# Kernel optimization log

Hardware: AMD Instinct MI355X
Metric: run time of the kernel (lower is better)

The kernel has to match this reference:

```python
import jax, jax.numpy as jnp
import numpy as np


def setup_inputs() -> dict:
    key = jax.random.key(0)
    k1, k2 = jax.random.split(key)
    x1 = jax.random.normal(k1, (256, 128, 32, 32), dtype=jnp.float32)   # queries [B,C,h,w]
    x2 = jax.random.normal(k2, (16, 8, 128, 32, 32), dtype=jnp.float32)  # supports [n_way,shot,C,h,w]
    return {"x1": x1, "x2": x2}


def reference(x1, x2):
    # --- cal_covariance: per-class channel covariance over all support pixels ---
    W, S, C, h, w = x2.shape
    sup = x2.transpose(0, 2, 1, 3, 4).reshape(W, C, S * h * w)  # [W, C, S*h*w]
    sup = sup - sup.mean(axis=2, keepdims=True)
    cova = jnp.einsum('wci,wdi->wcd', sup, sup) / (S * h * w - 1)  # [W, C, C]

    # --- cal_similarity: diagonal of q^T Cova q with per-channel L2-normalized query ---
    B, C, h, w = x1.shape
    q = x1.reshape(B, C, h * w)
    q = q / jnp.linalg.norm(q, axis=2, keepdims=True)  # norm over spatial dim per channel
    # diag_i = q[:, i]^T Cova q[:, i]; compute diagonal directly (no (hw)x(hw) matrix)
    sim = jnp.einsum('bci,wcd,bdi->bwi', q, cova, q)  # [B, W, h*w]
    return sim.reshape(B, W * h * w)
```

## Files before the change

kernel.cpp:

```cpp
#include <hip/hip_runtime.h>

typedef _Float16 half8 __attribute__((ext_vector_type(8)));
typedef _Float16 half4 __attribute__((ext_vector_type(4)));
typedef float    f32x4 __attribute__((ext_vector_type(4)));

#define W_CLS 16
#define SHOT  8
#define C_CH  128
#define HW    1024
#define NSAMP (SHOT*HW)
#define B_Q   256

__device__ __forceinline__ void gload_lds16(const _Float16* g, _Float16* l) {
    __builtin_amdgcn_global_load_lds((const __attribute__((address_space(1))) unsigned int*)g,
                                     (__attribute__((address_space(3))) unsigned int*)l,
                                     16, 0, 0);
}


__global__ __launch_bounds__(512) void cova_kernel(const float* __restrict__ x2,
                                                   float* __restrict__ PG,
                                                   float* __restrict__ pmean) {
    __shared__ _Float16 XT[2][128*72];
    __shared__ float mred[128][4];
    int tid = threadIdx.x;

    int w = blockIdx.x >> 4, ks = blockIdx.x & 15;
    int s = ks >> 1, p00 = (ks & 1) * 512;
    int c = tid >> 2, ph = (tid & 3) * 16;
    const float* src = x2 + (((size_t)(w*SHOT + s))*C_CH + c)*HW + p00 + ph;
    int lane = tid & 63, wv = tid >> 6;
    int lr = lane & 15, lg = lane >> 4;
    int mt0 = (wv & 3)*2, nt0 = (wv >> 2)*4;

    float msum = 0.f;
    f32x4 acc[2][4];
    #pragma unroll
    for (int mm = 0; mm < 2; ++mm)
        #pragma unroll
        for (int nn = 0; nn < 4; ++nn) acc[mm][nn] = (f32x4){0.f,0.f,0.f,0.f};

    float4 rg[4];
    #pragma unroll
    for (int j = 0; j < 4; ++j) rg[j] = *(const float4*)(src + j*4);
    #pragma unroll
    for (int j = 0; j < 4; ++j) {
        msum += rg[j].x + rg[j].y + rg[j].z + rg[j].w;
        half4 h = {(_Float16)rg[j].x, (_Float16)rg[j].y, (_Float16)rg[j].z, (_Float16)rg[j].w};
        *(half4*)(&XT[0][c*72 + ph + j*4]) = h;
    }
    __syncthreads();

    for (int ch = 0; ch < 8; ++ch) {
        int buf = ch & 1;
        if (ch < 7) {
            #pragma unroll
            for (int j = 0; j < 4; ++j) rg[j] = *(const float4*)(src + (ch+1)*64 + j*4);
        }
        const _Float16* xb = XT[buf];
        #pragma unroll
        for (int kk = 0; kk < 2; ++kk) {
            half8 Bv[4], Av[2];
            #pragma unroll
            for (int nn = 0; nn < 4; ++nn)
                Bv[nn] = *(const half8*)(xb + ((nt0+nn)*16 + lr)*72 + kk*32 + lg*8);
            #pragma unroll
            for (int mm = 0; mm < 2; ++mm)
                Av[mm] = *(const half8*)(xb + ((mt0+mm)*16 + lr)*72 + kk*32 + lg*8);
            #pragma unroll
            for (int mm = 0; mm < 2; ++mm)
                #pragma unroll
                for (int nn = 0; nn < 4; ++nn)
                    acc[mm][nn] = __builtin_amdgcn_mfma_f32_16x16x32_f16(Av[mm], Bv[nn], acc[mm][nn], 0,0,0);
        }
        if (ch < 7) {
            #pragma unroll
            for (int j = 0; j < 4; ++j) {
                msum += rg[j].x + rg[j].y + rg[j].z + rg[j].w;
                half4 h = {(_Float16)rg[j].x, (_Float16)rg[j].y, (_Float16)rg[j].z, (_Float16)rg[j].w};
                *(half4*)(&XT[buf^1][c*72 + ph + j*4]) = h;
            }
        }
        __syncthreads();
    }

    mred[c][tid & 3] = msum;
    __syncthreads();
    if (tid < 128)
        pmean[((size_t)w*16 + ks)*128 + tid] = mred[tid][0]+mred[tid][1]+mred[tid][2]+mred[tid][3];

    float* pg = PG + ((size_t)w*16 + ks)*16384;
    #pragma unroll
    for (int mm = 0; mm < 2; ++mm)
        #pragma unroll
        for (int nn = 0; nn < 4; ++nn)
            #pragma unroll
            for (int r = 0; r < 4; ++r) {
                int cr = (mt0+mm)*16 + lg*4 + r;
                int d  = (nt0+nn)*16 + lr;
                pg[cr*128 + d] = acc[mm][nn][r];
            }
}

__global__ __launch_bounds__(512) void qcr_kernel(const float* __restrict__ x1,
                                                  _Float16* __restrict__ qf,
                                                  const float* __restrict__ PG,
                                                  const float* __restrict__ pmean,
                                                  _Float16* __restrict__ Uh) {
    if (blockIdx.x >= 256) {
        __shared__ float ms[128];
        int t = threadIdx.x;
        int bid = blockIdx.x - 256;
        int w = bid >> 3, rg = bid & 7;
        if (t < 128) {
            float sum = 0.f;
            for (int ks = 0; ks < 16; ++ks) sum += pmean[((size_t)w*16 + ks)*128 + t];
            ms[t] = sum * (1.0f/NSAMP);
        }
        __syncthreads();
        const float* pg = PG + (size_t)w*16*16384;
        #pragma unroll
        for (int it = 0; it < 4; ++it) {
            int e = it*512 + t;
            int r = rg*16 + (e >> 7), d = e & 127;
            float g = 0.f;
            for (int ks = 0; ks < 16; ++ks) g += pg[(size_t)ks*16384 + r*128 + d];
            float val = (g - (float)NSAMP*ms[r]*ms[d]) * (1.0f/(NSAMP-1));
            float uval = (d > r) ? val : ((d == r) ? 0.5f*val : 0.0f);
            Uh[((size_t)w*128 + r)*128 + d] = (_Float16)uval;
        }
        return;
    }

    __shared__ _Float16 T[128*258];
    __shared__ float rnL[128];
    int tid = threadIdx.x, lane = tid & 63, wv = tid >> 6;
    int b = blockIdx.x;
    const float* xb = x1 + (size_t)b * C_CH * HW;

    #pragma unroll
    for (int cc = 0; cc < 16; ++cc) {
        int c = wv*16 + cc;
        const f32x4* row = (const f32x4*)(xb + (size_t)c * HW);
        float s = 0.f;
        #pragma unroll
        for (int j = 0; j < 4; ++j) {
            f32x4 v = row[lane + j*64];
            s += v[0]*v[0] + v[1]*v[1] + v[2]*v[2] + v[3]*v[3];
        }
        #pragma unroll
        for (int off = 32; off; off >>= 1) s += __shfl_xor(s, off, 64);
        if (lane == 0) rnL[c] = 1.0f / sqrtf(s);
    }
    __syncthreads();

    for (int ic = 0; ic < 4; ++ic) {
        #pragma unroll
        for (int cc = 0; cc < 16; ++cc) {
            int c = wv*16 + cc;
            f32x4 v = *(const f32x4*)(xb + (size_t)c * HW + ic*256 + lane*4);
            float sc = rnL[c];
            half4 h = {(_Float16)(v[0]*sc), (_Float16)(v[1]*sc),
                       (_Float16)(v[2]*sc), (_Float16)(v[3]*sc)};
            *(half4*)(&T[c*258 + lane*4]) = h;
        }
        __syncthreads();
        #pragma unroll
        for (int it = 0; it < 8; ++it) {
            int slot = it*512 + tid;
            int tl = slot >> 8;
            int kk = (slot >> 6) & 3;
            int ln = slot & 63;
            int i_loc = tl*16 + (ln & 15);
            int c0 = kk*32 + (ln >> 4)*8;
            half8 pk;
            #pragma unroll
            for (int e = 0; e < 8; ++e) pk[e] = T[(c0+e)*258 + i_loc];
            *(half8*)(qf + (((size_t)b*64 + ic*16 + tl)*4 + kk)*512 + ln*8) = pk;
        }
        __syncthreads();
    }
}

#define TR 4
__global__ __launch_bounds__(256, 3) void sim_kernel(const _Float16* __restrict__ qf,
                                                     const _Float16* __restrict__ Uh,
                                                     float* __restrict__ out) {
    __shared__ _Float16 stage[2][TR*2048];
    int tid = threadIdx.x, lane = tid & 63, wv = tid >> 6;
    int lr = lane & 15, lg = lane >> 4;
    int b = blockIdx.x & 255, wg = blockIdx.x >> 8;
    int w = wg*4 + wv;

    half8 A[20];
    {
        const _Float16* Ub = Uh + (size_t)w*C_CH*C_CH + (size_t)lr*C_CH + lg*8;
        int idx = 0;
        #pragma unroll
        for (int kk = 0; kk < 4; ++kk)
            #pragma unroll
            for (int m = 0; m <= 2*kk+1; ++m) {
                A[idx] = *(const half8*)(Ub + (size_t)m*16*C_CH + kk*32);
                ++idx;
            }
    }

    const _Float16* qfb = qf + (size_t)b * 131072;

    #pragma unroll
    for (int k = 0; k < 4; ++k)
        gload_lds16(qfb + tid*8 + k*2048, &stage[0][tid*8 + k*2048]);
    __syncthreads();

    int offD0 = (lg>>1)*128 + lr*8 + (lg&1)*4;
    float* ob = out + ((size_t)b*W_CLS + w)*HW;
    int cur = 0;

    for (int r = 0; r < 16; ++r) {
        if (r < 15) {
            const _Float16* gsrc = qfb + (size_t)(r+1)*(TR*2048);
            #pragma unroll
            for (int k = 0; k < 4; ++k)
                gload_lds16(gsrc + tid*8 + k*2048, &stage[cur^1][tid*8 + k*2048]);
        }
        #pragma unroll
        for (int ti = 0; ti < TR; ++ti) {
            const _Float16* gt = qfb + (size_t)(r*TR + ti)*2048;
            half4 D[8];
            #pragma unroll
            for (int m = 0; m < 8; ++m)
                D[m] = *(const half4*)(gt + (m>>1)*512 + (m&1)*256 + offD0);
            const _Float16* tb = &stage[cur][ti*2048];
            half8 B[4];
            #pragma unroll
            for (int kk = 0; kk < 4; ++kk)
                B[kk] = *(const half8*)(tb + kk*512 + lane*8);
            f32x4 acc[8];
            #pragma unroll
            for (int m = 0; m < 8; ++m) acc[m] = (f32x4){0.f,0.f,0.f,0.f};
            __builtin_amdgcn_s_setprio(1);
            {
                int idx = 0;
                #pragma unroll
                for (int kk = 0; kk < 4; ++kk)
                    #pragma unroll
                    for (int m = 0; m <= 2*kk+1; ++m) {
                        acc[m] = __builtin_amdgcn_mfma_f32_16x16x32_f16(A[idx], B[kk], acc[m], 0, 0, 0);
                        ++idx;
                    }
            }
            __builtin_amdgcn_s_setprio(0);
            float s = 0.f;
            #pragma unroll
            for (int m = 0; m < 8; ++m) {
                s = fmaf((float)D[m][0], acc[m][0], s);
                s = fmaf((float)D[m][1], acc[m][1], s);
                s = fmaf((float)D[m][2], acc[m][2], s);
                s = fmaf((float)D[m][3], acc[m][3], s);
            }
            s += __shfl_xor(s, 16, 64);
            s += __shfl_xor(s, 32, 64);
            if (lane < 16) ob[(r*TR + ti)*16 + lr] = 2.0f * s;
        }
        __syncthreads();
        cur ^= 1;
    }
}
#undef TR


__global__ __launch_bounds__(256) void rnorm_kernel(const float* __restrict__ x1,
                                                    float* __restrict__ rn) {
    int row  = blockIdx.x * 4 + (threadIdx.x >> 6);
    int lane = threadIdx.x & 63;
    const float4* p = (const float4*)(x1 + (size_t)row * HW);
    float s = 0.f;
    #pragma unroll
    for (int it = 0; it < 4; ++it) {
        float4 v = p[lane + it * 64];
        s += v.x*v.x + v.y*v.y + v.z*v.z + v.w*v.w;
    }
    for (int off = 32; off; off >>= 1) s += __shfl_down(s, off, 64);
    if (lane == 0) rn[row] = 1.0f / sqrtf(s);
}

__global__ __launch_bounds__(256) void mean_kernel_f(const float* __restrict__ x2,
                                                     float* __restrict__ mean) {
    int wc = blockIdx.x;
    int w  = wc >> 7, c = wc & 127;
    const float* base = x2 + ((size_t)(w * SHOT) * C_CH + c) * HW;
    int tid = threadIdx.x;
    float sum = 0.f;
    for (int s = 0; s < SHOT; ++s) {
        const float* row = base + (size_t)s * C_CH * HW;
        for (int p = tid; p < HW; p += 256) sum += row[p];
    }
    for (int off = 32; off; off >>= 1) sum += __shfl_down(sum, off, 64);
    __shared__ float red[4];
    int lane = tid & 63, wv = tid >> 6;
    if (lane == 0) red[wv] = sum;
    __syncthreads();
    if (tid == 0) mean[wc] = (red[0] + red[1] + red[2] + red[3]) * (1.0f / NSAMP);
}

__global__ __launch_bounds__(256) void cova_kernel_f(const float* __restrict__ x2,
                                                     const float* __restrict__ mean,
                                                     _Float16* __restrict__ covah) {
    int bid = blockIdx.x;
    int w  = bid >> 4;
    int c0 = ((bid >> 2) & 3) * 32;
    int d0 = (bid & 3) * 32;
    __shared__ float As[32][33];
    __shared__ float Bs[32][33];
    int tid = threadIdx.x;
    int ty = tid >> 4, tx = tid & 15;
    int lrr = tid >> 3, lc = (tid & 7) * 4;
    const float* base = x2 + (size_t)w * SHOT * C_CH * HW;
    float acc00 = 0.f, acc01 = 0.f, acc10 = 0.f, acc11 = 0.f;
    for (int k0 = 0; k0 < NSAMP; k0 += 32) {
        int s = k0 >> 10, p = k0 & 1023;
        const float4 a4 = *(const float4*)(base + ((size_t)s * C_CH + (c0 + lrr)) * HW + p + lc);
        const float4 b4 = *(const float4*)(base + ((size_t)s * C_CH + (d0 + lrr)) * HW + p + lc);
        As[lrr][lc+0] = a4.x; As[lrr][lc+1] = a4.y; As[lrr][lc+2] = a4.z; As[lrr][lc+3] = a4.w;
        Bs[lrr][lc+0] = b4.x; Bs[lrr][lc+1] = b4.y; Bs[lrr][lc+2] = b4.z; Bs[lrr][lc+3] = b4.w;
        __syncthreads();
        #pragma unroll
        for (int kk = 0; kk < 32; ++kk) {
            float a0 = As[ty*2][kk],   a1 = As[ty*2+1][kk];
            float b0 = Bs[tx*2][kk],   b1 = Bs[tx*2+1][kk];
            acc00 = fmaf(a0, b0, acc00);
            acc01 = fmaf(a0, b1, acc01);
            acc10 = fmaf(a1, b0, acc10);
            acc11 = fmaf(a1, b1, acc11);
        }
        __syncthreads();
    }
    const float inv = 1.0f / (NSAMP - 1);
    int c = c0 + ty * 2, d = d0 + tx * 2;
    float mc0 = mean[w*128 + c],     mc1 = mean[w*128 + c + 1];
    float md0 = mean[w*128 + d],     md1 = mean[w*128 + d + 1];
    _Float16* o = covah + ((size_t)w * 128 + c) * 128 + d;
    o[0]   = (_Float16)((acc00 - (float)NSAMP * mc0 * md0) * inv);
    o[1]   = (_Float16)((acc01 - (float)NSAMP * mc0 * md1) * inv);
    o[128] = (_Float16)((acc10 - (float)NSAMP * mc1 * md0) * inv);
    o[129] = (_Float16)((acc11 - (float)NSAMP * mc1 * md1) * inv);
}

#define LDQ 136
__global__ __launch_bounds__(512) void sim_kernel_f(const float* __restrict__ x1,
                                                    const _Float16* __restrict__ Ch,
                                                    const float* __restrict__ rn,
                                                    float* __restrict__ out) {
    __shared__ _Float16 qT[128][LDQ];
    __shared__ float simbuf[2][128];
    int tid = threadIdx.x;
    int bq  = blockIdx.x;
    int b   = bq >> 3;
    int i0  = (bq & 7) * 128;
    {
        int c  = tid >> 2;
        int iq = (tid & 3) * 32;
        const float* src = x1 + ((size_t)b * C_CH + c) * HW + i0 + iq;
        float scale = rn[b * C_CH + c];
        #pragma unroll
        for (int j4 = 0; j4 < 8; ++j4) {
            f32x4 v = *(const f32x4*)(src + j4 * 4);
            qT[iq + j4*4 + 0][c] = (_Float16)(v[0] * scale);
            qT[iq + j4*4 + 1][c] = (_Float16)(v[1] * scale);
            qT[iq + j4*4 + 2][c] = (_Float16)(v[2] * scale);
            qT[iq + j4*4 + 3][c] = (_Float16)(v[3] * scale);
        }
    }
    __syncthreads();
    int lane = tid & 63;
    int wv   = tid >> 6;
    int mh   = wv >> 2;
    int nq   = wv & 3;
    int d0w  = mh * 64;
    int iw   = nq * 32;
    int lr   = lane & 15;
    int lg   = lane >> 4;
    float qd[4][2][4];
    #pragma unroll
    for (int m = 0; m < 4; ++m)
        #pragma unroll
        for (int n = 0; n < 2; ++n) {
            half4 hq = *(const half4*)&qT[iw + n*16 + lr][d0w + m*16 + lg*4];
            qd[m][n][0] = (float)hq[0];
            qd[m][n][1] = (float)hq[1];
            qd[m][n][2] = (float)hq[2];
            qd[m][n][3] = (float)hq[3];
        }
    for (int w = 0; w < W_CLS; ++w) {
        const _Float16* Cw = Ch + (size_t)w * C_CH * C_CH;
        half8 A[4][4];
        #pragma unroll
        for (int m = 0; m < 4; ++m)
            #pragma unroll
            for (int k = 0; k < 4; ++k)
                A[m][k] = *(const half8*)(Cw + (size_t)(d0w + m*16 + lr) * C_CH + k*32 + lg*8);
        f32x4 acc[4][2];
        #pragma unroll
        for (int m = 0; m < 4; ++m)
            #pragma unroll
            for (int n = 0; n < 2; ++n)
                acc[m][n] = (f32x4){0.f, 0.f, 0.f, 0.f};
        #pragma unroll
        for (int k = 0; k < 4; ++k) {
            #pragma unroll
            for (int n = 0; n < 2; ++n) {
                half8 Bf = *(const half8*)&qT[iw + n*16 + lr][k*32 + lg*8];
                #pragma unroll
                for (int m = 0; m < 4; ++m)
                    acc[m][n] = __builtin_amdgcn_mfma_f32_16x16x32_f16(A[m][k], Bf, acc[m][n], 0, 0, 0);
            }
        }
        float s0 = 0.f, s1 = 0.f;
        #pragma unroll
        for (int m = 0; m < 4; ++m) {
            #pragma unroll
            for (int r = 0; r < 4; ++r) {
                s0 = fmaf(qd[m][0][r], acc[m][0][r], s0);
                s1 = fmaf(qd[m][1][r], acc[m][1][r], s1);
            }
        }
        s0 += __shfl_xor(s0, 16); s0 += __shfl_xor(s0, 32);
        s1 += __shfl_xor(s1, 16); s1 += __shfl_xor(s1, 32);
        if (lane < 16) {
            simbuf[mh][iw + 0*16 + lane] = s0;
            simbuf[mh][iw + 1*16 + lane] = s1;
        }
        __syncthreads();
        if (tid < 128)
            out[((size_t)b * W_CLS + w) * HW + i0 + tid] = simbuf[0][tid] + simbuf[1][tid];
        __syncthreads();
    }
}


extern "C" void kernel_launch(void* const* d_in, const int* in_sizes, int n_in,
                              void* d_out, int out_size, void* d_ws, size_t ws_size,
                              hipStream_t stream) {
    (void)in_sizes; (void)n_in; (void)out_size;
    const float* x1 = (const float*)d_in[0];
    const float* x2 = (const float*)d_in[1];
    float* out = (float*)d_out;

    char* ws = (char*)d_ws;
    const size_t OFF_QF  = 0;
    const size_t OFF_PG  = 67108864;
    const size_t OFF_PM  = OFF_PG  + 16777216;
    const size_t OFF_UH  = OFF_PM  + 131072;
    const size_t OFF_RN  = OFF_UH  + 524288;
    const size_t NEED    = OFF_RN  + 131072;

    if (ws_size >= NEED) {
        _Float16* qf  = (_Float16*)(ws + OFF_QF);
        float*    PG  = (float*)(ws + OFF_PG);
        float*    pm  = (float*)(ws + OFF_PM);
        _Float16* Uh  = (_Float16*)(ws + OFF_UH);
        cova_kernel<<<256,  512, 0, stream>>>(x2, PG, pm);
        qcr_kernel <<<384,  512, 0, stream>>>(x1, qf, PG, pm, Uh);
        sim_kernel <<<1024, 256, 0, stream>>>(qf, Uh, out);
    } else {
        float*    mean = (float*)ws;
        float*    rn   = mean + W_CLS*C_CH;
        _Float16* Ch   = (_Float16*)(rn + B_Q*C_CH);
        mean_kernel_f<<<W_CLS*C_CH,  256, 0, stream>>>(x2, mean);
        cova_kernel_f<<<W_CLS*16,    256, 0, stream>>>(x2, mean, Ch);
        rnorm_kernel <<<B_Q*C_CH/4,  256, 0, stream>>>(x1, rn);
        sim_kernel_f <<<B_Q*8,       512, 0, stream>>>(x1, Ch, rn, out);
    }
}
```

Baseline: 175.2 us.

## Merge query prep with covariance partials and split out covariance reduction

The query normalization and transpose work now runs in the same launch as the support covariance partial GEMMs, filling the GPU with 512 blocks instead of 256. Because the PG reduction depends on the covariance partials, it moves into its own small kernel that runs after that launch. The sim kernel also reads its diagonal query operand from the LDS stage buffer it already staged, instead of reloading it from global memory. In exchange, one big block now uses 65KB of shared memory for both roles, which could reduce occupancy for the covariance blocks.

```diff
diff --git a/kernel.cpp b/kernel.cpp
--- a/kernel.cpp
+++ b/kernel.cpp
@@ -18,14 +18,71 @@
 }
 
 
-__global__ __launch_bounds__(512) void cova_kernel(const float* __restrict__ x2,
-                                                   float* __restrict__ PG,
-                                                   float* __restrict__ pmean) {
-    __shared__ _Float16 XT[2][128*72];
-    __shared__ float mred[128][4];
+__global__ __launch_bounds__(512) void helper_kernel(const float* __restrict__ x1,
+                                                     const float* __restrict__ x2,
+                                                     float* __restrict__ PG,
+                                                     float* __restrict__ pmean,
+                                                     _Float16* __restrict__ qf) {
+    __shared__ __align__(16) char smem[66560];
     int tid = threadIdx.x;
 
-    int w = blockIdx.x >> 4, ks = blockIdx.x & 15;
+    if (blockIdx.x < 256) {
+        _Float16* T   = (_Float16*)smem;
+        float*    rnL = (float*)(smem + 66048);
+        int lane = tid & 63, wv = tid >> 6;
+        int b = blockIdx.x;
+        const float* xb = x1 + (size_t)b * C_CH * HW;
+
+        #pragma unroll
+        for (int cc = 0; cc < 16; ++cc) {
+            int c = wv*16 + cc;
+            const f32x4* row = (const f32x4*)(xb + (size_t)c * HW);
+            float s = 0.f;
+            #pragma unroll
+            for (int j = 0; j < 4; ++j) {
+                f32x4 v = row[lane + j*64];
+                s += v[0]*v[0] + v[1]*v[1] + v[2]*v[2] + v[3]*v[3];
+            }
+            #pragma unroll
+            for (int off = 32; off; off >>= 1) s += __shfl_xor(s, off, 64);
+            if (lane == 0) rnL[c] = 1.0f / sqrtf(s);
+        }
+        __syncthreads();
+
+        for (int ic = 0; ic < 4; ++ic) {
+            #pragma unroll
+            for (int cc = 0; cc < 16; ++cc) {
+                int c = wv*16 + cc;
+                f32x4 v = *(const f32x4*)(xb + (size_t)c * HW + ic*256 + lane*4);
+                float sc = rnL[c];
+                half4 h = {(_Float16)(v[0]*sc), (_Float16)(v[1]*sc),
+                           (_Float16)(v[2]*sc), (_Float16)(v[3]*sc)};
+                *(half4*)(&T[c*258 + lane*4]) = h;
+            }
+            __syncthreads();
+            #pragma unroll
+            for (int it = 0; it < 8; ++it) {
+                int slot = it*512 + tid;
+                int tl = slot >> 8;
+                int kk = (slot >> 6) & 3;
+                int ln = slot & 63;
+                int i_loc = tl*16 + (ln & 15);
+                int c0 = kk*32 + (ln >> 4)*8;
+                half8 pk;
+                #pragma unroll
+                for (int e = 0; e < 8; ++e) pk[e] = T[(c0+e)*258 + i_loc];
+                *(half8*)(qf + (((size_t)b*64 + ic*16 + tl)*4 + kk)*512 + ln*8) = pk;
+            }
+            __syncthreads();
+        }
+        return;
+    }
+
+    _Float16* XT   = (_Float16*)smem;
+    float (*mred)[4] = (float(*)[4])(smem + 36864);
+
+    int bid = blockIdx.x - 256;
+    int w = bid >> 4, ks = bid & 15;
     int s = ks >> 1, p00 = (ks & 1) * 512;
     int c = tid >> 2, ph = (tid & 3) * 16;
     const float* src = x2 + (((size_t)(w*SHOT + s))*C_CH + c)*HW + p00 + ph;
@@ -47,7 +104,7 @@
     for (int j = 0; j < 4; ++j) {
         msum += rg[j].x + rg[j].y + rg[j].z + rg[j].w;
         half4 h = {(_Float16)rg[j].x, (_Float16)rg[j].y, (_Float16)rg[j].z, (_Float16)rg[j].w};
-        *(half4*)(&XT[0][c*72 + ph + j*4]) = h;
+        *(half4*)(&XT[c*72 + ph + j*4]) = h;
     }
     __syncthreads();
 
@@ -57,7 +114,7 @@
             #pragma unroll
             for (int j = 0; j < 4; ++j) rg[j] = *(const float4*)(src + (ch+1)*64 + j*4);
         }
-        const _Float16* xb = XT[buf];
+        const _Float16* xb = XT + buf*(128*72);
         #pragma unroll
         for (int kk = 0; kk < 2; ++kk) {
             half8 Bv[4], Av[2];
@@ -78,7 +135,7 @@
             for (int j = 0; j < 4; ++j) {
                 msum += rg[j].x + rg[j].y + rg[j].z + rg[j].w;
                 half4 h = {(_Float16)rg[j].x, (_Float16)rg[j].y, (_Float16)rg[j].z, (_Float16)rg[j].w};
-                *(half4*)(&XT[buf^1][c*72 + ph + j*4]) = h;
+                *(half4*)(&XT[(buf^1)*(128*72) + c*72 + ph + j*4]) = h;
             }
         }
         __syncthreads();
@@ -102,83 +159,28 @@
             }
 }
 
-__global__ __launch_bounds__(512) void qcr_kernel(const float* __restrict__ x1,
-                                                  _Float16* __restrict__ qf,
-                                                  const float* __restrict__ PG,
-                                                  const float* __restrict__ pmean,
-                                                  _Float16* __restrict__ Uh) {
-    if (blockIdx.x >= 256) {
-        __shared__ float ms[128];
-        int t = threadIdx.x;
-        int bid = blockIdx.x - 256;
-        int w = bid >> 3, rg = bid & 7;
-        if (t < 128) {
-            float sum = 0.f;
-            for (int ks = 0; ks < 16; ++ks) sum += pmean[((size_t)w*16 + ks)*128 + t];
-            ms[t] = sum * (1.0f/NSAMP);
-        }
-        __syncthreads();
-        const float* pg = PG + (size_t)w*16*16384;
-        #pragma unroll
-        for (int it = 0; it < 4; ++it) {
-            int e = it*512 + t;
-            int r = rg*16 + (e >> 7), d = e & 127;
-            float g = 0.f;
-            for (int ks = 0; ks < 16; ++ks) g += pg[(size_t)ks*16384 + r*128 + d];
-            float val = (g - (float)NSAMP*ms[r]*ms[d]) * (1.0f/(NSAMP-1));
-            float uval = (d > r) ? val : ((d == r) ? 0.5f*val : 0.0f);
-            Uh[((size_t)w*128 + r)*128 + d] = (_Float16)uval;
-        }
-        return;
-    }
-
-    __shared__ _Float16 T[128*258];
-    __shared__ float rnL[128];
-    int tid = threadIdx.x, lane = tid & 63, wv = tid >> 6;
-    int b = blockIdx.x;
-    const float* xb = x1 + (size_t)b * C_CH * HW;
-
-    #pragma unroll
-    for (int cc = 0; cc < 16; ++cc) {
-        int c = wv*16 + cc;
-        const f32x4* row = (const f32x4*)(xb + (size_t)c * HW);
-        float s = 0.f;
-        #pragma unroll
-        for (int j = 0; j < 4; ++j) {
-            f32x4 v = row[lane + j*64];
-            s += v[0]*v[0] + v[1]*v[1] + v[2]*v[2] + v[3]*v[3];
-        }
-        #pragma unroll
-        for (int off = 32; off; off >>= 1) s += __shfl_xor(s, off, 64);
-        if (lane == 0) rnL[c] = 1.0f / sqrtf(s);
-    }
-    __syncthreads();
-
-    for (int ic = 0; ic < 4; ++ic) {
-        #pragma unroll
-        for (int cc = 0; cc < 16; ++cc) {
-            int c = wv*16 + cc;
-            f32x4 v = *(const f32x4*)(xb + (size_t)c * HW + ic*256 + lane*4);
-            float sc = rnL[c];
-            half4 h = {(_Float16)(v[0]*sc), (_Float16)(v[1]*sc),
-                       (_Float16)(v[2]*sc), (_Float16)(v[3]*sc)};
-            *(half4*)(&T[c*258 + lane*4]) = h;
-        }
-        __syncthreads();
-        #pragma unroll
-        for (int it = 0; it < 8; ++it) {
-            int slot = it*512 + tid;
-            int tl = slot >> 8;
-            int kk = (slot >> 6) & 3;
-            int ln = slot & 63;
-            int i_loc = tl*16 + (ln & 15);
-            int c0 = kk*32 + (ln >> 4)*8;
-            half8 pk;
-            #pragma unroll
-            for (int e = 0; e < 8; ++e) pk[e] = T[(c0+e)*258 + i_loc];
-            *(half8*)(qf + (((size_t)b*64 + ic*16 + tl)*4 + kk)*512 + ln*8) = pk;
-        }
-        __syncthreads();
+__global__ __launch_bounds__(256) void cova_reduce(const float* __restrict__ PG,
+                                                   const float* __restrict__ pmean,
+                                                   _Float16* __restrict__ Uh) {
+    __shared__ float ms[128];
+    int t = threadIdx.x;
+    int w = blockIdx.x >> 3, rg = blockIdx.x & 7;
+    if (t < 128) {
+        float sum = 0.f;
+        for (int ks = 0; ks < 16; ++ks) sum += pmean[((size_t)w*16 + ks)*128 + t];
+        ms[t] = sum * (1.0f/NSAMP);
+    }
+    __syncthreads();
+    const float* pg = PG + (size_t)w*16*16384;
+    #pragma unroll
+    for (int it = 0; it < 8; ++it) {
+        int e = it*256 + t;
+        int r = rg*16 + (e >> 7), d = e & 127;
+        float g = 0.f;
+        for (int ks = 0; ks < 16; ++ks) g += pg[(size_t)ks*16384 + r*128 + d];
+        float val = (g - (float)NSAMP*ms[r]*ms[d]) * (1.0f/(NSAMP-1));
+        float uval = (d > r) ? val : ((d == r) ? 0.5f*val : 0.0f);
+        Uh[((size_t)w*128 + r)*128 + d] = (_Float16)uval;
     }
 }
 
@@ -225,16 +227,15 @@
         }
         #pragma unroll
         for (int ti = 0; ti < TR; ++ti) {
-            const _Float16* gt = qfb + (size_t)(r*TR + ti)*2048;
-            half4 D[8];
-            #pragma unroll
-            for (int m = 0; m < 8; ++m)
-                D[m] = *(const half4*)(gt + (m>>1)*512 + (m&1)*256 + offD0);
             const _Float16* tb = &stage[cur][ti*2048];
             half8 B[4];
             #pragma unroll
             for (int kk = 0; kk < 4; ++kk)
                 B[kk] = *(const half8*)(tb + kk*512 + lane*8);
+            half4 D[8];
+            #pragma unroll
+            for (int m = 0; m < 8; ++m)
+                D[m] = *(const half4*)(tb + (m>>1)*512 + (m&1)*256 + offD0);
             f32x4 acc[8];
             #pragma unroll
             for (int m = 0; m < 8; ++m) acc[m] = (f32x4){0.f,0.f,0.f,0.f};
@@ -459,9 +460,9 @@
         float*    PG  = (float*)(ws + OFF_PG);
         float*    pm  = (float*)(ws + OFF_PM);
         _Float16* Uh  = (_Float16*)(ws + OFF_UH);
-        cova_kernel<<<256,  512, 0, stream>>>(x2, PG, pm);
-        qcr_kernel <<<384,  512, 0, stream>>>(x1, qf, PG, pm, Uh);
-        sim_kernel <<<1024, 256, 0, stream>>>(qf, Uh, out);
+        helper_kernel<<<512,  512, 0, stream>>>(x1, x2, PG, pm, qf);
+        cova_reduce  <<<128,  256, 0, stream>>>(PG, pm, Uh);
+        sim_kernel   <<<1024, 256, 0, stream>>>(qf, Uh, out);
     } else {
         float*    mean = (float*)ws;
         float*    rn   = mean + W_CLS*C_CH;
```

Measured after the change: 190.0 us. 1.08x slower.
